# Optimization experiments

Hardware: AMD Instinct MI355X
Metric: run time of the kernel (lower is better)

## Reference

```python
import jax, jax.numpy as jnp
import numpy as np

DIM = 768
HEADS = 12
HIDDEN = 4 * DIM
B, N = 8, 1024
EPS = 1e-5


def setup_inputs() -> dict:
    key = jax.random.key(0)
    ks = jax.random.split(key, 8)
    s = 0.02
    return {
        "x": jax.random.normal(ks[0], (B, N, DIM), dtype=jnp.float32),
        "ln1_g": jnp.ones((DIM,), jnp.float32),
        "ln1_b": jnp.zeros((DIM,), jnp.float32),
        "qkv_w": jax.random.normal(ks[1], (3 * DIM, DIM), jnp.float32) * s,
        "proj_w": jax.random.normal(ks[2], (DIM, DIM), jnp.float32) * s,
        "proj_b": jnp.zeros((DIM,), jnp.float32),
        "ln2_g": jnp.ones((DIM,), jnp.float32),
        "ln2_b": jnp.zeros((DIM,), jnp.float32),
        "fc1_w": jax.random.normal(ks[3], (HIDDEN, DIM), jnp.float32) * s,
        "fc1_b": jnp.zeros((HIDDEN,), jnp.float32),
        "fc2_w": jax.random.normal(ks[4], (DIM, HIDDEN), jnp.float32) * s,
        "fc2_b": jnp.zeros((DIM,), jnp.float32),
    }


def _layernorm(x, g, b):
    mu = jnp.mean(x, axis=-1, keepdims=True)
    var = jnp.mean(jnp.square(x - mu), axis=-1, keepdims=True)
    return (x - mu) * jax.lax.rsqrt(var + EPS) * g + b


def reference(x, ln1_g, ln1_b, qkv_w, proj_w, proj_b, ln2_g, ln2_b, fc1_w, fc1_b, fc2_w, fc2_b):
    Bn, Nn, C = x.shape
    H = HEADS
    D = C // H
    scale = D ** -0.5

    # --- attention branch ---
    h = _layernorm(x, ln1_g, ln1_b)
    qkv = h @ qkv_w.T                      # [B,N,3C] (qkv_bias=False)
    qkv = qkv.reshape(Bn, Nn, 3, H, D)
    q = qkv[:, :, 0].transpose(0, 2, 1, 3)  # [B,H,N,D]
    k = qkv[:, :, 1].transpose(0, 2, 1, 3)
    v = qkv[:, :, 2].transpose(0, 2, 1, 3)
    attn = jnp.einsum('bhnd,bhmd->bhnm', q, k) * scale  # [B,H,N,N]
    attn = jax.nn.softmax(attn, axis=-1)
    ctx = jnp.einsum('bhnm,bhmd->bhnd', attn, v)         # [B,H,N,D]
    ctx = ctx.transpose(0, 2, 1, 3).reshape(Bn, Nn, C)
    x = x + ctx @ proj_w.T + proj_b

    # --- MLP branch ---
    h = _layernorm(x, ln2_g, ln2_b)
    h = jax.nn.gelu(h @ fc1_w.T + fc1_b, approximate=False)
    return x + h @ fc2_w.T + fc2_b
```

## Files before the change

### kernel.cpp

```cpp
#include <hip/hip_runtime.h>
#include <cstdint>

typedef __attribute__((ext_vector_type(8))) short short8;
typedef __attribute__((ext_vector_type(4))) float f32x4;
typedef unsigned short u16t;

__device__ __forceinline__ u16t f2bf(float f) {
  uint32_t u = __float_as_uint(f);
  u += 0x7fffu + ((u >> 16) & 1u);
  return (u16t)(u >> 16);
}

__device__ __forceinline__ uint32_t cvtpk(float lo, float hi) {
  uint32_t r;
  asm("v_cvt_pk_bf16_f32 %0, %1, %2" : "=v"(r) : "v"(lo), "v"(hi));
  return r;
}

__device__ __forceinline__ void gload_lds16(const void* g, void* l) {
  __builtin_amdgcn_global_load_lds(
      (const __attribute__((address_space(1))) void*)g,
      (__attribute__((address_space(3))) void*)l, 16, 0, 0);
}

__global__ __launch_bounds__(256) void cvt_bf16_kernel(const float* __restrict__ in,
                                                       u16t* __restrict__ out, int n8) {
  int i = blockIdx.x * 256 + threadIdx.x;
  if (i >= n8) return;
  const float4* p = (const float4*)in + (size_t)i * 2;
  float4 a = p[0], b = p[1];
  union { short8 v; u16t e[8]; } r;
  r.e[0] = f2bf(a.x); r.e[1] = f2bf(a.y); r.e[2] = f2bf(a.z); r.e[3] = f2bf(a.w);
  r.e[4] = f2bf(b.x); r.e[5] = f2bf(b.y); r.e[6] = f2bf(b.z); r.e[7] = f2bf(b.w);
  *((short8*)out + i) = r.v;
}

__global__ __launch_bounds__(256) void ln_kernel(const float* __restrict__ x,
                                                 const float* __restrict__ g,
                                                 const float* __restrict__ b,
                                                 u16t* __restrict__ out) {
  int row = blockIdx.x, tid = threadIdx.x;
  int wave = tid >> 6, lane = tid & 63;
  const float* xr = x + (size_t)row * 768;
  float v0 = xr[tid], v1 = xr[tid + 256], v2 = xr[tid + 512];
  float s = v0 + v1 + v2;
  float q = v0 * v0 + v1 * v1 + v2 * v2;
#pragma unroll
  for (int m = 32; m >= 1; m >>= 1) {
    s += __shfl_xor(s, m, 64);
    q += __shfl_xor(q, m, 64);
  }
  __shared__ float red[8];
  if (lane == 0) { red[wave] = s; red[4 + wave] = q; }
  __syncthreads();
  s = red[0] + red[1] + red[2] + red[3];
  q = red[4] + red[5] + red[6] + red[7];
  float mu = s * (1.0f / 768.0f);
  float var = q * (1.0f / 768.0f) - mu * mu;
  float rs = rsqrtf(var + 1e-5f);
  u16t* orow = out + (size_t)row * 768;
  orow[tid]       = f2bf((v0 - mu) * rs * g[tid]       + b[tid]);
  orow[tid + 256] = f2bf((v1 - mu) * rs * g[tid + 256] + b[tid + 256]);
  orow[tid + 512] = f2bf((v2 - mu) * rs * g[tid + 512] + b[tid + 512]);
}

template <int EPI, int BM, int MINB>
__global__ __launch_bounds__(256, MINB) void gemm_bt(const u16t* __restrict__ A,
                                                     const u16t* __restrict__ W,
                                                     void* __restrict__ Cout,
                                                     const float* __restrict__ bias,
                                                     const float* __restrict__ res,
                                                     int M, int N, int K) {
  __shared__ __align__(16) u16t As[2][BM * 64];
  __shared__ __align__(16) u16t Bs[2][128 * 64];
  constexpr int MF = BM / 32;
  int tid = threadIdx.x;
  int wave = tid >> 6, lane = tid & 63;
  int wr = wave >> 1, wc = wave & 1;
  int q = lane & 15, g = lane >> 4;
  int bm = blockIdx.y * BM;
  int bn = blockIdx.x * 128;
  f32x4 acc[MF][4] = {};

  int lr = lane >> 3, lc = lane & 7;
  const u16t* Abase = A + (size_t)(bm + lr) * K + ((lc ^ lr) * 8);
  const u16t* Wbase = W + (size_t)(bn + lr) * K + ((lc ^ lr) * 8);

  auto stage = [&](int kt, int db) {
#pragma unroll
    for (int i = 0; i < BM / 32; i++) {
      int chunk = wave * (BM / 32) + i;
      gload_lds16(Abase + (size_t)(chunk * 8) * K + kt, (void*)(As[db] + chunk * 512));
    }
#pragma unroll
    for (int i = 0; i < 4; i++) {
      int chunk = wave * 4 + i;
      gload_lds16(Wbase + (size_t)(chunk * 8) * K + kt, (void*)(Bs[db] + chunk * 512));
    }
  };

  stage(0, 0);
  __syncthreads();

  int NT = K >> 6;
  for (int t = 0; t < NT; ++t) {
    int db = t & 1;
    if (t + 1 < NT) stage((t + 1) * 64, db ^ 1);
    const u16t* Ab = As[db];
    const u16t* Bb = Bs[db];

    short8 af[MF][2], bfr[4][2];
#pragma unroll
    for (int m = 0; m < MF; m++) {
      int row = wr * (BM / 2) + m * 16 + q;
#pragma unroll
      for (int s = 0; s < 2; s++)
        af[m][s] = *(const short8*)(Ab + row * 64 + (((s * 4 + g) ^ (row & 7)) * 8));
    }
#pragma unroll
    for (int n = 0; n < 4; n++) {
      int row = wc * 64 + n * 16 + q;
#pragma unroll
      for (int s = 0; s < 2; s++)
        bfr[n][s] = *(const short8*)(Bb + row * 64 + (((s * 4 + g) ^ (row & 7)) * 8));
    }
    __builtin_amdgcn_s_setprio(1);
#pragma unroll
    for (int m = 0; m < MF; m++)
#pragma unroll
      for (int n = 0; n < 4; n++) {
        acc[m][n] = __builtin_amdgcn_mfma_f32_16x16x32_bf16(bfr[n][0], af[m][0], acc[m][n], 0, 0, 0);
        acc[m][n] = __builtin_amdgcn_mfma_f32_16x16x32_bf16(bfr[n][1], af[m][1], acc[m][n], 0, 0, 0);
      }
    __builtin_amdgcn_s_setprio(0);
    __syncthreads();
  }

#pragma unroll
  for (int m = 0; m < MF; m++) {
    int r = bm + wr * (BM / 2) + m * 16 + q;
#pragma unroll
    for (int n = 0; n < 4; n++) {
      int c = bn + wc * 64 + n * 16 + g * 4;
      f32x4 v = acc[m][n];
      if constexpr (EPI == 0) {
        uint2 pk = make_uint2(cvtpk(v[0], v[1]), cvtpk(v[2], v[3]));
        *(uint2*)((u16t*)Cout + (size_t)r * N + c) = pk;
      } else if constexpr (EPI == 1) {
        const float4 bv = *(const float4*)(bias + c);
        const float4 rv = *(const float4*)(res + (size_t)r * N + c);
        float4 o;
        o.x = v[0] + bv.x + rv.x; o.y = v[1] + bv.y + rv.y;
        o.z = v[2] + bv.z + rv.z; o.w = v[3] + bv.w + rv.w;
        *(float4*)((float*)Cout + (size_t)r * N + c) = o;
      } else {
        const float4 bv = *(const float4*)(bias + c);
        float t0 = v[0] + bv.x, t1 = v[1] + bv.y, t2 = v[2] + bv.z, t3 = v[3] + bv.w;
        t0 = 0.5f * t0 * (1.0f + erff(t0 * 0.70710678118f));
        t1 = 0.5f * t1 * (1.0f + erff(t1 * 0.70710678118f));
        t2 = 0.5f * t2 * (1.0f + erff(t2 * 0.70710678118f));
        t3 = 0.5f * t3 * (1.0f + erff(t3 * 0.70710678118f));
        uint2 pk = make_uint2(cvtpk(t0, t1), cvtpk(t2, t3));
        *(uint2*)((u16t*)Cout + (size_t)r * N + c) = pk;
      }
    }
  }
}

__global__ __launch_bounds__(256) void vtrans_kernel(const u16t* __restrict__ qkv,
                                                     u16t* __restrict__ vt) {
  __shared__ u16t T[64][66];
  int h = blockIdx.x % 12, bb = blockIdx.x / 12, kt = blockIdx.y * 64;
  int t = threadIdx.x;
  int r = t >> 2, dc = t & 3;
  const u16t* src = qkv + (size_t)(bb * 1024 + kt + r) * 2304 + 1536 + h * 64 + dc * 16;
  union { uint4 u[2]; u16t e[16]; uint32_t w[8]; } buf;
  buf.u[0] = *(const uint4*)src;
  buf.u[1] = *(const uint4*)(src + 8);
#pragma unroll
  for (int j = 0; j < 8; j++)
    *(uint32_t*)&T[r][dc * 16 + 2 * j] = buf.w[j];
  __syncthreads();
  int d = t >> 2, kc = t & 3;
  union { uint4 u[2]; u16t e[16]; } o;
#pragma unroll
  for (int j = 0; j < 16; j++) o.e[j] = T[kc * 16 + j][d];
  u16t* dst = vt + ((size_t)blockIdx.x * 64 + d) * 1024 + kt + kc * 16;
  *(uint4*)dst = o.u[0];
  *(uint4*)(dst + 8) = o.u[1];
}

__global__ __launch_bounds__(256, 3) void attn_kernel(const u16t* __restrict__ qkv,
                                                      const u16t* __restrict__ vt,
                                                      u16t* __restrict__ ctx) {
  __shared__ __align__(16) u16t Ks[2][64 * 64];
  __shared__ __align__(16) u16t Vs[2][64 * 64];
  __shared__ __align__(16) u16t Plds[4][32 * 72];
  int tid = threadIdx.x;
  int wave = tid >> 6, lane = tid & 63;
  int q = lane & 15, g = lane >> 4;

  int bid = blockIdx.x;
  int xcd = bid & 7, j = bid >> 3;
  int head = xcd + 8 * (j >> 3);
  int qt = (j & 7) * 128 + wave * 32;
  int b = head / 12, h = head % 12;

  const u16t* base = qkv + (size_t)b * 1024 * 2304 + h * 64;
  const u16t* kbase = base + 768;
  const u16t* vtb = vt + (size_t)head * 64 * 1024;

  short8 qf[2][2];
#pragma unroll
  for (int hf = 0; hf < 2; hf++)
#pragma unroll
    for (int hh = 0; hh < 2; hh++)
      qf[hf][hh] = *(const short8*)(base + (size_t)(qt + hf * 16 + q) * 2304 + hh * 32 + g * 8);

  int lr = lane >> 3, lc = lane & 7;
  const u16t* ksrc = kbase + (size_t)lr * 2304 + (size_t)((lc ^ lr) * 8);
  const u16t* vsrc = vtb + (size_t)lr * 1024 + (size_t)((lc ^ lr) * 8);
  int c0 = wave * 2, c1 = wave * 2 + 1;

  auto stage = [&](int kt, int buf) {
    gload_lds16(ksrc + (size_t)(kt + c0 * 8) * 2304, (void*)(Ks[buf] + c0 * 512));
    gload_lds16(ksrc + (size_t)(kt + c1 * 8) * 2304, (void*)(Ks[buf] + c1 * 512));
    gload_lds16(vsrc + (size_t)(c0 * 8) * 1024 + kt, (void*)(Vs[buf] + c0 * 512));
    gload_lds16(vsrc + (size_t)(c1 * 8) * 1024 + kt, (void*)(Vs[buf] + c1 * 512));
  };

  float mA = -1e30f, mB = -1e30f, lA = 0.f, lB = 0.f;
  f32x4 oA[4] = {}, oB[4] = {};
  u16t* Pw = Plds[wave];

  stage(0, 0);
  __syncthreads();

  for (int t = 0; t < 16; ++t) {
    int buf = t & 1;
    if (t < 15) stage((t + 1) * 64, buf ^ 1);

    const u16t* Kb = Ks[buf];
    const u16t* Vb = Vs[buf];

    f32x4 sA[4] = {}, sB[4] = {};
    __builtin_amdgcn_s_setprio(1);
#pragma unroll
    for (int n = 0; n < 4; n++) {
      int row = n * 16 + q;
      short8 k0 = *(const short8*)(Kb + row * 64 + ((g ^ (q & 7)) * 8));
      short8 k1 = *(const short8*)(Kb + row * 64 + (((4 + g) ^ (q & 7)) * 8));
      sA[n] = __builtin_amdgcn_mfma_f32_16x16x32_bf16(k0, qf[0][0], sA[n], 0, 0, 0);
      sA[n] = __builtin_amdgcn_mfma_f32_16x16x32_bf16(k1, qf[0][1], sA[n], 0, 0, 0);
      sB[n] = __builtin_amdgcn_mfma_f32_16x16x32_bf16(k0, qf[1][0], sB[n], 0, 0, 0);
      sB[n] = __builtin_amdgcn_mfma_f32_16x16x32_bf16(k1, qf[1][1], sB[n], 0, 0, 0);
    }
    __builtin_amdgcn_s_setprio(0);

    float alphaA, alphaB;
    {
      float t0 = fmaxf(fmaxf(sA[0][0], sA[0][1]), fmaxf(sA[0][2], sA[0][3]));
      float t1 = fmaxf(fmaxf(sA[1][0], sA[1][1]), fmaxf(sA[1][2], sA[1][3]));
      float t2 = fmaxf(fmaxf(sA[2][0], sA[2][1]), fmaxf(sA[2][2], sA[2][3]));
      float t3 = fmaxf(fmaxf(sA[3][0], sA[3][1]), fmaxf(sA[3][2], sA[3][3]));
      float tm = fmaxf(fmaxf(t0, t1), fmaxf(t2, t3));
      tm = fmaxf(tm, __shfl_xor(tm, 16, 64));
      tm = fmaxf(tm, __shfl_xor(tm, 32, 64));
      float mnew = fmaxf(mA, tm);
      alphaA = __expf((mA - mnew) * 0.125f);
      mA = mnew;
#pragma unroll
      for (int n = 0; n < 4; n++)
#pragma unroll
        for (int i = 0; i < 4; i++) sA[n][i] = __expf((sA[n][i] - mnew) * 0.125f);
      float r0 = (sA[0][0] + sA[0][1]) + (sA[0][2] + sA[0][3]);
      float r1 = (sA[1][0] + sA[1][1]) + (sA[1][2] + sA[1][3]);
      float r2 = (sA[2][0] + sA[2][1]) + (sA[2][2] + sA[2][3]);
      float r3 = (sA[3][0] + sA[3][1]) + (sA[3][2] + sA[3][3]);
      float rs = (r0 + r1) + (r2 + r3);
      rs += __shfl_xor(rs, 16, 64);
      rs += __shfl_xor(rs, 32, 64);
      lA = lA * alphaA + rs;
#pragma unroll
      for (int n = 0; n < 4; n++) {
        uint32_t w0 = cvtpk(sA[n][0], sA[n][1]);
        uint32_t w1 = cvtpk(sA[n][2], sA[n][3]);
        *(uint2*)(Pw + q * 72 + n * 16 + g * 4) = make_uint2(w0, w1);
      }
    }
    {
      float t0 = fmaxf(fmaxf(sB[0][0], sB[0][1]), fmaxf(sB[0][2], sB[0][3]));
      float t1 = fmaxf(fmaxf(sB[1][0], sB[1][1]), fmaxf(sB[1][2], sB[1][3]));
      float t2 = fmaxf(fmaxf(sB[2][0], sB[2][1]), fmaxf(sB[2][2], sB[2][3]));
      float t3 = fmaxf(fmaxf(sB[3][0], sB[3][1]), fmaxf(sB[3][2], sB[3][3]));
      float tm = fmaxf(fmaxf(t0, t1), fmaxf(t2, t3));
      tm = fmaxf(tm, __shfl_xor(tm, 16, 64));
      tm = fmaxf(tm, __shfl_xor(tm, 32, 64));
      float mnew = fmaxf(mB, tm);
      alphaB = __expf((mB - mnew) * 0.125f);
      mB = mnew;
#pragma unroll
      for (int n = 0; n < 4; n++)
#pragma unroll
        for (int i = 0; i < 4; i++) sB[n][i] = __expf((sB[n][i] - mnew) * 0.125f);
      float r0 = (sB[0][0] + sB[0][1]) + (sB[0][2] + sB[0][3]);
      float r1 = (sB[1][0] + sB[1][1]) + (sB[1][2] + sB[1][3]);
      float r2 = (sB[2][0] + sB[2][1]) + (sB[2][2] + sB[2][3]);
      float r3 = (sB[3][0] + sB[3][1]) + (sB[3][2] + sB[3][3]);
      float rs = (r0 + r1) + (r2 + r3);
      rs += __shfl_xor(rs, 16, 64);
      rs += __shfl_xor(rs, 32, 64);
      lB = lB * alphaB + rs;
#pragma unroll
      for (int n = 0; n < 4; n++) {
        uint32_t w0 = cvtpk(sB[n][0], sB[n][1]);
        uint32_t w1 = cvtpk(sB[n][2], sB[n][3]);
        *(uint2*)(Pw + (16 + q) * 72 + n * 16 + g * 4) = make_uint2(w0, w1);
      }
    }

#pragma unroll
    for (int n = 0; n < 4; n++)
#pragma unroll
      for (int i = 0; i < 4; i++) {
        oA[n][i] *= alphaA;
        oB[n][i] *= alphaB;
      }

    short8 pA[2], pB[2];
#pragma unroll
    for (int hh = 0; hh < 2; hh++) {
      pA[hh] = *(const short8*)(Pw + q * 72 + hh * 32 + g * 8);
      pB[hh] = *(const short8*)(Pw + (16 + q) * 72 + hh * 32 + g * 8);
    }
    __builtin_amdgcn_s_setprio(1);
#pragma unroll
    for (int n = 0; n < 4; n++) {
      int row = n * 16 + q;
      short8 v0 = *(const short8*)(Vb + row * 64 + ((g ^ (q & 7)) * 8));
      short8 v1 = *(const short8*)(Vb + row * 64 + (((4 + g) ^ (q & 7)) * 8));
      oA[n] = __builtin_amdgcn_mfma_f32_16x16x32_bf16(v0, pA[0], oA[n], 0, 0, 0);
      oA[n] = __builtin_amdgcn_mfma_f32_16x16x32_bf16(v1, pA[1], oA[n], 0, 0, 0);
      oB[n] = __builtin_amdgcn_mfma_f32_16x16x32_bf16(v0, pB[0], oB[n], 0, 0, 0);
      oB[n] = __builtin_amdgcn_mfma_f32_16x16x32_bf16(v1, pB[1], oB[n], 0, 0, 0);
    }
    __builtin_amdgcn_s_setprio(0);

    __syncthreads();
  }

  float invA = 1.f / lA, invB = 1.f / lB;
  u16t* crowA = ctx + (size_t)(b * 1024 + qt + q) * 768 + h * 64;
  u16t* crowB = ctx + (size_t)(b * 1024 + qt + 16 + q) * 768 + h * 64;
#pragma unroll
  for (int n = 0; n < 4; n++) {
    uint32_t a0 = (uint32_t)f2bf(oA[n][0] * invA) | ((uint32_t)f2bf(oA[n][1] * invA) << 16);
    uint32_t a1 = (uint32_t)f2bf(oA[n][2] * invA) | ((uint32_t)f2bf(oA[n][3] * invA) << 16);
    *(uint32_t*)(crowA + n * 16 + g * 4) = a0;
    *(uint32_t*)(crowA + n * 16 + g * 4 + 2) = a1;
    uint32_t b0 = (uint32_t)f2bf(oB[n][0] * invB) | ((uint32_t)f2bf(oB[n][1] * invB) << 16);
    uint32_t b1 = (uint32_t)f2bf(oB[n][2] * invB) | ((uint32_t)f2bf(oB[n][3] * invB) << 16);
    *(uint32_t*)(crowB + n * 16 + g * 4) = b0;
    *(uint32_t*)(crowB + n * 16 + g * 4 + 2) = b1;
  }
}

extern "C" void kernel_launch(void* const* d_in, const int* in_sizes, int n_in,
                              void* d_out, int out_size, void* d_ws, size_t ws_size,
                              hipStream_t stream) {
  const float* x      = (const float*)d_in[0];
  const float* ln1_g  = (const float*)d_in[1];
  const float* ln1_b  = (const float*)d_in[2];
  const float* qkv_w  = (const float*)d_in[3];
  const float* proj_w = (const float*)d_in[4];
  const float* proj_b = (const float*)d_in[5];
  const float* ln2_g  = (const float*)d_in[6];
  const float* ln2_b  = (const float*)d_in[7];
  const float* fc1_w  = (const float*)d_in[8];
  const float* fc1_b  = (const float*)d_in[9];
  const float* fc2_w  = (const float*)d_in[10];
  const float* fc2_b  = (const float*)d_in[11];

  char* ws = (char*)d_ws;
  u16t* h1   = (u16t*)(ws + 0);
  u16t* qkvb = (u16t*)(ws + 12582912);
  u16t* ctx  = (u16t*)(ws + 50331648);
  float* x2  = (float*)(ws + 62914560);
  u16t* hid  = (u16t*)(ws + 88080384);
  u16t* wq   = (u16t*)(ws + 138412032);
  u16t* wp   = (u16t*)(ws + 141950976);
  u16t* w1   = (u16t*)(ws + 143130624);
  u16t* w2   = (u16t*)(ws + 147849216);
  u16t* vtb  = h1;
  float* out = (float*)d_out;

  cvt_bf16_kernel<<<864, 256, 0, stream>>>(qkv_w, wq, 221184);
  cvt_bf16_kernel<<<288, 256, 0, stream>>>(proj_w, wp, 73728);
  cvt_bf16_kernel<<<1152, 256, 0, stream>>>(fc1_w, w1, 294912);
  cvt_bf16_kernel<<<1152, 256, 0, stream>>>(fc2_w, w2, 294912);

  ln_kernel<<<8192, 256, 0, stream>>>(x, ln1_g, ln1_b, h1);
  gemm_bt<0, 128, 2><<<dim3(18, 64), 256, 0, stream>>>(h1, wq, qkvb, nullptr, nullptr, 8192, 2304, 768);
  vtrans_kernel<<<dim3(96, 16), 256, 0, stream>>>(qkvb, vtb);
  attn_kernel<<<768, 256, 0, stream>>>(qkvb, vtb, ctx);
  gemm_bt<1, 64, 3><<<dim3(6, 128), 256, 0, stream>>>(ctx, wp, x2, proj_b, x, 8192, 768, 768);
  ln_kernel<<<8192, 256, 0, stream>>>(x2, ln2_g, ln2_b, h1);
  gemm_bt<2, 128, 2><<<dim3(24, 64), 256, 0, stream>>>(h1, w1, hid, fc1_b, nullptr, 8192, 3072, 768);
  gemm_bt<1, 64, 3><<<dim3(6, 128), 256, 0, stream>>>(hid, w2, out, fc2_b, x2, 8192, 768, 3072);
}
```

Before: 287.4 us.

## Use triple-buffered LDS pipeline with XCD-aware tile mapping in all GEMMs

Replaces the templated double-buffered GEMM with a single 64x128-tile kernel that keeps two K-tiles of global-to-LDS loads in flight through a three-stage buffer ring. It waits with an explicit vmcnt and a single barrier per iteration instead of a trailing syncthreads. It also linearizes the grid and remaps block IDs so consecutive tiles are spread across the eight XCDs, aiming for better L2 locality. The QKV and FC1 GEMMs drop from 128-row to 64-row tiles, which reduces reuse per block in exchange for deeper prefetch and more blocks.

```diff
diff --git a/kernel.cpp b/kernel.cpp
--- a/kernel.cpp
+++ b/kernel.cpp
@@ -64,23 +64,27 @@
   orow[tid + 512] = f2bf((v2 - mu) * rs * g[tid + 512] + b[tid + 512]);
 }
 
-template <int EPI, int BM, int MINB>
-__global__ __launch_bounds__(256, MINB) void gemm_bt(const u16t* __restrict__ A,
-                                                     const u16t* __restrict__ W,
-                                                     void* __restrict__ Cout,
-                                                     const float* __restrict__ bias,
-                                                     const float* __restrict__ res,
-                                                     int M, int N, int K) {
-  __shared__ __align__(16) u16t As[2][BM * 64];
-  __shared__ __align__(16) u16t Bs[2][128 * 64];
-  constexpr int MF = BM / 32;
+template <int EPI>
+__global__ __launch_bounds__(256, 2) void gemm_p2(const u16t* __restrict__ A,
+                                                  const u16t* __restrict__ W,
+                                                  void* __restrict__ Cout,
+                                                  const float* __restrict__ bias,
+                                                  const float* __restrict__ res,
+                                                  int N, int K) {
+  __shared__ __align__(16) u16t As[3][64 * 64];
+  __shared__ __align__(16) u16t Bs[3][128 * 64];
   int tid = threadIdx.x;
   int wave = tid >> 6, lane = tid & 63;
   int wr = wave >> 1, wc = wave & 1;
   int q = lane & 15, g = lane >> 4;
-  int bm = blockIdx.y * BM;
-  int bn = blockIdx.x * 128;
-  f32x4 acc[MF][4] = {};
+
+  int nwg = gridDim.x;
+  int bid = blockIdx.x;
+  int T = (bid & 7) * (nwg >> 3) + (bid >> 3);
+  int bm = (T & 127) * 64;
+  int bn = (T >> 7) * 128;
+
+  f32x4 acc[2][4] = {};
 
   int lr = lane >> 3, lc = lane & 7;
   const u16t* Abase = A + (size_t)(bm + lr) * K + ((lc ^ lr) * 8);
@@ -88,8 +92,8 @@
 
   auto stage = [&](int kt, int db) {
 #pragma unroll
-    for (int i = 0; i < BM / 32; i++) {
-      int chunk = wave * (BM / 32) + i;
+    for (int i = 0; i < 2; i++) {
+      int chunk = wave * 2 + i;
       gload_lds16(Abase + (size_t)(chunk * 8) * K + kt, (void*)(As[db] + chunk * 512));
     }
 #pragma unroll
@@ -100,19 +104,26 @@
   };
 
   stage(0, 0);
-  __syncthreads();
+  stage(64, 1);
 
   int NT = K >> 6;
   for (int t = 0; t < NT; ++t) {
-    int db = t & 1;
-    if (t + 1 < NT) stage((t + 1) * 64, db ^ 1);
+    int db = t % 3;
+    if (t + 1 < NT) {
+      asm volatile("s_waitcnt vmcnt(6)" ::: "memory");
+    } else {
+      asm volatile("s_waitcnt vmcnt(0)" ::: "memory");
+    }
+    __builtin_amdgcn_s_barrier();
+    __builtin_amdgcn_sched_barrier(0);
+    if (t + 2 < NT) stage((t + 2) * 64, (t + 2) % 3);
+
     const u16t* Ab = As[db];
     const u16t* Bb = Bs[db];
-
-    short8 af[MF][2], bfr[4][2];
-#pragma unroll
-    for (int m = 0; m < MF; m++) {
-      int row = wr * (BM / 2) + m * 16 + q;
+    short8 af[2][2], bfr[4][2];
+#pragma unroll
+    for (int m = 0; m < 2; m++) {
+      int row = wr * 32 + m * 16 + q;
 #pragma unroll
       for (int s = 0; s < 2; s++)
         af[m][s] = *(const short8*)(Ab + row * 64 + (((s * 4 + g) ^ (row & 7)) * 8));
@@ -126,19 +137,18 @@
     }
     __builtin_amdgcn_s_setprio(1);
 #pragma unroll
-    for (int m = 0; m < MF; m++)
+    for (int m = 0; m < 2; m++)
 #pragma unroll
       for (int n = 0; n < 4; n++) {
         acc[m][n] = __builtin_amdgcn_mfma_f32_16x16x32_bf16(bfr[n][0], af[m][0], acc[m][n], 0, 0, 0);
         acc[m][n] = __builtin_amdgcn_mfma_f32_16x16x32_bf16(bfr[n][1], af[m][1], acc[m][n], 0, 0, 0);
       }
     __builtin_amdgcn_s_setprio(0);
-    __syncthreads();
   }
 
 #pragma unroll
-  for (int m = 0; m < MF; m++) {
-    int r = bm + wr * (BM / 2) + m * 16 + q;
+  for (int m = 0; m < 2; m++) {
+    int r = bm + wr * 32 + m * 16 + q;
 #pragma unroll
     for (int n = 0; n < 4; n++) {
       int c = bn + wc * 64 + n * 16 + g * 4;
@@ -400,11 +410,11 @@
   cvt_bf16_kernel<<<1152, 256, 0, stream>>>(fc2_w, w2, 294912);
 
   ln_kernel<<<8192, 256, 0, stream>>>(x, ln1_g, ln1_b, h1);
-  gemm_bt<0, 128, 2><<<dim3(18, 64), 256, 0, stream>>>(h1, wq, qkvb, nullptr, nullptr, 8192, 2304, 768);
+  gemm_p2<0><<<2304, 256, 0, stream>>>(h1, wq, qkvb, nullptr, nullptr, 2304, 768);
   vtrans_kernel<<<dim3(96, 16), 256, 0, stream>>>(qkvb, vtb);
   attn_kernel<<<768, 256, 0, stream>>>(qkvb, vtb, ctx);
-  gemm_bt<1, 64, 3><<<dim3(6, 128), 256, 0, stream>>>(ctx, wp, x2, proj_b, x, 8192, 768, 768);
+  gemm_p2<1><<<768, 256, 0, stream>>>(ctx, wp, x2, proj_b, x, 768, 768);
   ln_kernel<<<8192, 256, 0, stream>>>(x2, ln2_g, ln2_b, h1);
-  gemm_bt<2, 128, 2><<<dim3(24, 64), 256, 0, stream>>>(h1, w1, hid, fc1_b, nullptr, 8192, 3072, 768);
-  gemm_bt<1, 64, 3><<<dim3(6, 128), 256, 0, stream>>>(hid, w2, out, fc2_b, x2, 8192, 768, 3072);
-}
+  gemm_p2<2><<<3072, 256, 0, stream>>>(h1, w1, hid, fc1_b, nullptr, 3072, 768);
+  gemm_p2<1><<<768, 256, 0, stream>>>(hid, w2, out, fc2_b, x2, 768, 3072);
+}
```

Result: slower. 369.0 us (+28.4%).

## Replace double-buffered GEMM with larger single-buffer tiles and swizzled 1D grid

Applied to the files above, without the earlier changes.

Replaces the templated double-buffered GEMM with two single-buffered variants: a 512-thread 128x256-tile kernel for the QKV and FC1 projections and a 256-thread 128x128-tile kernel for the proj and FC2 GEMMs. Both use a 1D grid with an XCD-style block swizzle. The aim is more reuse per tile, higher occupancy from the smaller LDS footprint, and better L2 locality. The cost is that global loads no longer overlap MFMA compute within a block, so latency hiding relies on other resident blocks.

```diff
diff --git a/kernel.cpp b/kernel.cpp
--- a/kernel.cpp
+++ b/kernel.cpp
@@ -21,6 +21,10 @@
   __builtin_amdgcn_global_load_lds(
       (const __attribute__((address_space(1))) void*)g,
       (__attribute__((address_space(3))) void*)l, 16, 0, 0);
+}
+
+__device__ __forceinline__ float gelu_exact(float v) {
+  return 0.5f * v * (1.0f + erff(v * 0.70710678118f));
 }
 
 __global__ __launch_bounds__(256) void cvt_bf16_kernel(const float* __restrict__ in,
@@ -64,69 +68,65 @@
   orow[tid + 512] = f2bf((v2 - mu) * rs * g[tid + 512] + b[tid + 512]);
 }
 
-template <int EPI, int BM, int MINB>
-__global__ __launch_bounds__(256, MINB) void gemm_bt(const u16t* __restrict__ A,
-                                                     const u16t* __restrict__ W,
-                                                     void* __restrict__ Cout,
-                                                     const float* __restrict__ bias,
-                                                     const float* __restrict__ res,
-                                                     int M, int N, int K) {
-  __shared__ __align__(16) u16t As[2][BM * 64];
-  __shared__ __align__(16) u16t Bs[2][128 * 64];
-  constexpr int MF = BM / 32;
+template <int EPI>
+__global__ __launch_bounds__(512, 3) void gemm5(const u16t* __restrict__ A,
+                                                const u16t* __restrict__ W,
+                                                void* __restrict__ Cout,
+                                                const float* __restrict__ bias,
+                                                const float* __restrict__ res,
+                                                int N, int K, int nbm) {
+  __shared__ __align__(16) u16t As[128 * 64];
+  __shared__ __align__(16) u16t Bs[256 * 64];
   int tid = threadIdx.x;
-  int wave = tid >> 6, lane = tid & 63;
-  int wr = wave >> 1, wc = wave & 1;
+  int wid = tid >> 6, lane = tid & 63;
+  int wr = wid >> 2, wc = wid & 3;
   int q = lane & 15, g = lane >> 4;
-  int bm = blockIdx.y * BM;
-  int bn = blockIdx.x * 128;
-  f32x4 acc[MF][4] = {};
+
+  int total = gridDim.x;
+  int bid = blockIdx.x;
+  int swz = (bid & 7) * (total >> 3) + (bid >> 3);
+  int bm = (swz % nbm) * 128;
+  int bn = (swz / nbm) * 256;
+
+  f32x4 acc[4][4] = {};
 
   int lr = lane >> 3, lc = lane & 7;
   const u16t* Abase = A + (size_t)(bm + lr) * K + ((lc ^ lr) * 8);
   const u16t* Wbase = W + (size_t)(bn + lr) * K + ((lc ^ lr) * 8);
 
-  auto stage = [&](int kt, int db) {
-#pragma unroll
-    for (int i = 0; i < BM / 32; i++) {
-      int chunk = wave * (BM / 32) + i;
-      gload_lds16(Abase + (size_t)(chunk * 8) * K + kt, (void*)(As[db] + chunk * 512));
-    }
-#pragma unroll
-    for (int i = 0; i < 4; i++) {
-      int chunk = wave * 4 + i;
-      gload_lds16(Wbase + (size_t)(chunk * 8) * K + kt, (void*)(Bs[db] + chunk * 512));
-    }
-  };
-
-  stage(0, 0);
-  __syncthreads();
-
   int NT = K >> 6;
   for (int t = 0; t < NT; ++t) {
-    int db = t & 1;
-    if (t + 1 < NT) stage((t + 1) * 64, db ^ 1);
-    const u16t* Ab = As[db];
-    const u16t* Bb = Bs[db];
-
-    short8 af[MF][2], bfr[4][2];
-#pragma unroll
-    for (int m = 0; m < MF; m++) {
-      int row = wr * (BM / 2) + m * 16 + q;
+    int kt = t * 64;
+#pragma unroll
+    for (int i = 0; i < 2; i++) {
+      int chunk = wid * 2 + i;
+      gload_lds16(Abase + (size_t)(chunk * 8) * K + kt, (void*)(As + chunk * 512));
+    }
+#pragma unroll
+    for (int i = 0; i < 4; i++) {
+      int chunk = wid * 4 + i;
+      gload_lds16(Wbase + (size_t)(chunk * 8) * K + kt, (void*)(Bs + chunk * 512));
+    }
+    __syncthreads();
+
+    short8 af[4][2], bfr[4][2];
+#pragma unroll
+    for (int m = 0; m < 4; m++) {
+      int row = wr * 64 + m * 16 + q;
 #pragma unroll
       for (int s = 0; s < 2; s++)
-        af[m][s] = *(const short8*)(Ab + row * 64 + (((s * 4 + g) ^ (row & 7)) * 8));
+        af[m][s] = *(const short8*)(As + row * 64 + (((s * 4 + g) ^ (row & 7)) * 8));
     }
 #pragma unroll
     for (int n = 0; n < 4; n++) {
       int row = wc * 64 + n * 16 + q;
 #pragma unroll
       for (int s = 0; s < 2; s++)
-        bfr[n][s] = *(const short8*)(Bb + row * 64 + (((s * 4 + g) ^ (row & 7)) * 8));
+        bfr[n][s] = *(const short8*)(Bs + row * 64 + (((s * 4 + g) ^ (row & 7)) * 8));
     }
     __builtin_amdgcn_s_setprio(1);
 #pragma unroll
-    for (int m = 0; m < MF; m++)
+    for (int m = 0; m < 4; m++)
 #pragma unroll
       for (int n = 0; n < 4; n++) {
         acc[m][n] = __builtin_amdgcn_mfma_f32_16x16x32_bf16(bfr[n][0], af[m][0], acc[m][n], 0, 0, 0);
@@ -137,8 +137,8 @@
   }
 
 #pragma unroll
-  for (int m = 0; m < MF; m++) {
-    int r = bm + wr * (BM / 2) + m * 16 + q;
+  for (int m = 0; m < 4; m++) {
+    int r = bm + wr * 64 + m * 16 + q;
 #pragma unroll
     for (int n = 0; n < 4; n++) {
       int c = bn + wc * 64 + n * 16 + g * 4;
@@ -155,12 +155,99 @@
         *(float4*)((float*)Cout + (size_t)r * N + c) = o;
       } else {
         const float4 bv = *(const float4*)(bias + c);
-        float t0 = v[0] + bv.x, t1 = v[1] + bv.y, t2 = v[2] + bv.z, t3 = v[3] + bv.w;
-        t0 = 0.5f * t0 * (1.0f + erff(t0 * 0.70710678118f));
-        t1 = 0.5f * t1 * (1.0f + erff(t1 * 0.70710678118f));
-        t2 = 0.5f * t2 * (1.0f + erff(t2 * 0.70710678118f));
-        t3 = 0.5f * t3 * (1.0f + erff(t3 * 0.70710678118f));
-        uint2 pk = make_uint2(cvtpk(t0, t1), cvtpk(t2, t3));
+        uint2 pk = make_uint2(cvtpk(gelu_exact(v[0] + bv.x), gelu_exact(v[1] + bv.y)),
+                              cvtpk(gelu_exact(v[2] + bv.z), gelu_exact(v[3] + bv.w)));
+        *(uint2*)((u16t*)Cout + (size_t)r * N + c) = pk;
+      }
+    }
+  }
+}
+
+template <int EPI>
+__global__ __launch_bounds__(256, 4) void gemm4(const u16t* __restrict__ A,
+                                                const u16t* __restrict__ W,
+                                                void* __restrict__ Cout,
+                                                const float* __restrict__ bias,
+                                                const float* __restrict__ res,
+                                                int N, int K, int nbm) {
+  __shared__ __align__(16) u16t As[128 * 64];
+  __shared__ __align__(16) u16t Bs[128 * 64];
+  int tid = threadIdx.x;
+  int wave = tid >> 6, lane = tid & 63;
+  int wr = wave >> 1, wc = wave & 1;
+  int q = lane & 15, g = lane >> 4;
+
+  int total = gridDim.x;
+  int bid = blockIdx.x;
+  int swz = (bid & 7) * (total >> 3) + (bid >> 3);
+  int bm = (swz % nbm) * 128;
+  int bn = (swz / nbm) * 128;
+
+  f32x4 acc[4][4] = {};
+
+  int lr = lane >> 3, lc = lane & 7;
+  const u16t* Abase = A + (size_t)(bm + lr) * K + ((lc ^ lr) * 8);
+  const u16t* Wbase = W + (size_t)(bn + lr) * K + ((lc ^ lr) * 8);
+
+  int NT = K >> 6;
+  for (int t = 0; t < NT; ++t) {
+    int kt = t * 64;
+#pragma unroll
+    for (int i = 0; i < 4; i++) {
+      int chunk = wave * 4 + i;
+      gload_lds16(Abase + (size_t)(chunk * 8) * K + kt, (void*)(As + chunk * 512));
+      gload_lds16(Wbase + (size_t)(chunk * 8) * K + kt, (void*)(Bs + chunk * 512));
+    }
+    __syncthreads();
+
+    short8 af[4][2], bfr[4][2];
+#pragma unroll
+    for (int m = 0; m < 4; m++) {
+      int row = wr * 64 + m * 16 + q;
+#pragma unroll
+      for (int s = 0; s < 2; s++)
+        af[m][s] = *(const short8*)(As + row * 64 + (((s * 4 + g) ^ (row & 7)) * 8));
+    }
+#pragma unroll
+    for (int n = 0; n < 4; n++) {
+      int row = wc * 64 + n * 16 + q;
+#pragma unroll
+      for (int s = 0; s < 2; s++)
+        bfr[n][s] = *(const short8*)(Bs + row * 64 + (((s * 4 + g) ^ (row & 7)) * 8));
+    }
+    __builtin_amdgcn_s_setprio(1);
+#pragma unroll
+    for (int m = 0; m < 4; m++)
+#pragma unroll
+      for (int n = 0; n < 4; n++) {
+        acc[m][n] = __builtin_amdgcn_mfma_f32_16x16x32_bf16(bfr[n][0], af[m][0], acc[m][n], 0, 0, 0);
+        acc[m][n] = __builtin_amdgcn_mfma_f32_16x16x32_bf16(bfr[n][1], af[m][1], acc[m][n], 0, 0, 0);
+      }
+    __builtin_amdgcn_s_setprio(0);
+    __syncthreads();
+  }
+
+#pragma unroll
+  for (int m = 0; m < 4; m++) {
+    int r = bm + wr * 64 + m * 16 + q;
+#pragma unroll
+    for (int n = 0; n < 4; n++) {
+      int c = bn + wc * 64 + n * 16 + g * 4;
+      f32x4 v = acc[m][n];
+      if constexpr (EPI == 0) {
+        uint2 pk = make_uint2(cvtpk(v[0], v[1]), cvtpk(v[2], v[3]));
+        *(uint2*)((u16t*)Cout + (size_t)r * N + c) = pk;
+      } else if constexpr (EPI == 1) {
+        const float4 bv = *(const float4*)(bias + c);
+        const float4 rv = *(const float4*)(res + (size_t)r * N + c);
+        float4 o;
+        o.x = v[0] + bv.x + rv.x; o.y = v[1] + bv.y + rv.y;
+        o.z = v[2] + bv.z + rv.z; o.w = v[3] + bv.w + rv.w;
+        *(float4*)((float*)Cout + (size_t)r * N + c) = o;
+      } else {
+        const float4 bv = *(const float4*)(bias + c);
+        uint2 pk = make_uint2(cvtpk(gelu_exact(v[0] + bv.x), gelu_exact(v[1] + bv.y)),
+                              cvtpk(gelu_exact(v[2] + bv.z), gelu_exact(v[3] + bv.w)));
         *(uint2*)((u16t*)Cout + (size_t)r * N + c) = pk;
       }
     }
@@ -400,11 +487,11 @@
   cvt_bf16_kernel<<<1152, 256, 0, stream>>>(fc2_w, w2, 294912);
 
   ln_kernel<<<8192, 256, 0, stream>>>(x, ln1_g, ln1_b, h1);
-  gemm_bt<0, 128, 2><<<dim3(18, 64), 256, 0, stream>>>(h1, wq, qkvb, nullptr, nullptr, 8192, 2304, 768);
+  gemm5<0><<<576, 512, 0, stream>>>(h1, wq, qkvb, nullptr, nullptr, 2304, 768, 64);
   vtrans_kernel<<<dim3(96, 16), 256, 0, stream>>>(qkvb, vtb);
   attn_kernel<<<768, 256, 0, stream>>>(qkvb, vtb, ctx);
-  gemm_bt<1, 64, 3><<<dim3(6, 128), 256, 0, stream>>>(ctx, wp, x2, proj_b, x, 8192, 768, 768);
+  gemm4<1><<<384, 256, 0, stream>>>(ctx, wp, x2, proj_b, x, 768, 768, 64);
   ln_kernel<<<8192, 256, 0, stream>>>(x2, ln2_g, ln2_b, h1);
-  gemm_bt<2, 128, 2><<<dim3(24, 64), 256, 0, stream>>>(h1, w1, hid, fc1_b, nullptr, 8192, 3072, 768);
-  gemm_bt<1, 64, 3><<<dim3(6, 128), 256, 0, stream>>>(hid, w2, out, fc2_b, x2, 8192, 768, 3072);
-}
+  gemm5<2><<<768, 512, 0, stream>>>(h1, w1, hid, fc1_b, nullptr, 3072, 768, 64);
+  gemm4<1><<<384, 256, 0, stream>>>(hid, w2, out, fc2_b, x2, 768, 3072, 64);
+}
```

New measurement: 488.2 us. +69.9%, slower.
